# Performance work log

Hardware: AMD Instinct MI355X
Metric: run time of the kernel (lower is better)

Reference implementation:

```python
import jax, jax.numpy as jnp
import numpy as np
from jax import lax

HEADS = 8
DIM_HEAD = 64
SCALE = DIM_HEAD ** -0.5

def conv2d(x, w, stride=1, pad=0):
    return lax.conv_general_dilated(
        x, w, window_strides=(stride, stride),
        padding=[(pad, pad), (pad, pad)],
        dimension_numbers=("NCHW", "OIHW", "NCHW"))

def setup_inputs() -> dict:
    key = jax.random.key(0)
    ks = jax.random.split(key, 5)
    b, dim, H, W = 8, 256, 32, 32
    inner = HEADS * DIM_HEAD  # 512
    x = jax.random.normal(ks[0], (b, dim, H, W), jnp.float32)
    Wq = jax.random.normal(ks[1], (inner, dim, 1, 1), jnp.float32) * 0.05
    Wkv = jax.random.normal(ks[2], (2 * inner, dim, 3, 3), jnp.float32) * 0.05
    Wout = jax.random.normal(ks[3], (dim, inner, 1, 1), jnp.float32) * 0.05
    bout = jnp.zeros((dim,), jnp.float32)
    return {"x": x, "Wq": Wq, "Wkv": Wkv, "Wout": Wout, "bout": bout}

def reference(x, Wq, Wkv, Wout, bout):
    b = x.shape[0]
    h, d = HEADS, DIM_HEAD
    q = conv2d(x, Wq, stride=1, pad=0)        # [b, h*d, H, W]
    kv = conv2d(x, Wkv, stride=1, pad=1)      # [b, 2*h*d, H, W]
    k, v = jnp.split(kv, 2, axis=1)
    out_h, out_w = q.shape[-2:]

    def to_bhnd(t):
        # b (h d) x y -> b h (x y) d
        B, _, X, Y = t.shape
        return t.reshape(B, h, d, X * Y).transpose(0, 1, 3, 2)

    q, k, v = map(to_bhnd, (q, k, v))
    dots = jnp.einsum("bhid,bhjd->bhij", q, k) * SCALE
    attn = jax.nn.softmax(dots, axis=-1)
    out = jnp.einsum("bhij,bhjd->bhid", attn, v)  # [b, h, n, d]
    # b h (x y) d -> b (h d) x y
    out = out.transpose(0, 1, 3, 2).reshape(b, h * d, out_h, out_w)
    out = jax.nn.gelu(out, approximate=False)
    out = conv2d(out, Wout, stride=1, pad=0) + bout[None, :, None, None]
    return out
```

## Files before the change

### kernel.cpp

```cpp
#include <hip/hip_runtime.h>
#include <math.h>

#define BATCH 8
#define DIM   256
#define NPIX  1024
#define DHEAD 64
#define INNER 512
#define KVCH  1024
#define PPIX  1156

typedef _Float16 half8 __attribute__((ext_vector_type(8)));
typedef _Float16 half4 __attribute__((ext_vector_type(4)));
typedef float    f32x4 __attribute__((ext_vector_type(4)));
typedef float    f32x16 __attribute__((ext_vector_type(16)));
#define MFMA16(a, b, c) __builtin_amdgcn_mfma_f32_16x16x32_f16(a, b, c, 0, 0, 0)
#define MFMA32(a, b, c) __builtin_amdgcn_mfma_f32_32x32x16_f16(a, b, c, 0, 0, 0)

static __device__ __forceinline__ float gelu_f(float v) {
    return 0.5f * v * (1.0f + erff(v * 0.70710678118654752440f));
}

static __device__ __forceinline__ void gload16(const _Float16* g, _Float16* l) {
    __builtin_amdgcn_global_load_lds(
        (const __attribute__((address_space(1))) unsigned int*)g,
        (__attribute__((address_space(3))) unsigned int*)l, 16, 0, 0);
}

__global__ __launch_bounds__(256) void prep_kernel(
    const float* __restrict__ Wq, const float* __restrict__ Wkv,
    const float* __restrict__ Wout, const float* __restrict__ x,
    _Float16* __restrict__ Aq, _Float16* __restrict__ Akv,
    _Float16* __restrict__ Aout, _Float16* __restrict__ xtp)
{
    const int bid = blockIdx.x, tid = threadIdx.x;
    if (bid < 512) {
        __shared__ float ts[64][65];
        const int pt = (bid & 15) * 64, ic0 = ((bid >> 4) & 3) * 64, b = bid >> 6;
        const float* xb = x + (((size_t)(b * DIM + ic0)) << 10) + pt;
#pragma unroll
        for (int e = tid; e < 4096; e += 256) {
            int i = e >> 6, p = e & 63;
            ts[i][p] = xb[((size_t)i << 10) + p];
        }
        __syncthreads();
#pragma unroll
        for (int e = tid; e < 512; e += 256) {
            int p = e >> 3, ig = e & 7;
            int gp = pt + p, y = gp >> 5, xc = gp & 31;
            half8 v;
#pragma unroll
            for (int u = 0; u < 8; ++u) v[u] = (_Float16)ts[ig * 8 + u][p];
            *(half8*)&xtp[((size_t)b * PPIX + (y + 1) * 34 + xc + 1) * 256 + ic0 + ig * 8] = v;
        }
    } else if (bid < 1024) {
        const int e = (bid - 512) * 256 + tid;
        Aq[e] = (_Float16)Wq[e];
    } else if (bid < 2048) {
        __shared__ float slab[2304];
        const int oc = bid - 1024;
        const float* src = Wkv + (size_t)oc * 2304;
#pragma unroll
        for (int j = tid; j < 2304; j += 256) slab[j] = src[j];
        __syncthreads();
        _Float16* dst = Akv + (size_t)oc * 2304;
#pragma unroll
        for (int j = tid; j < 2304; j += 256) {
            const int ic = j & 255, s = j >> 8;
            dst[j] = (_Float16)slab[ic * 9 + s];
        }
    } else if (bid < 2560) {
        const int e = (bid - 2048) * 256 + tid;
        Aout[e] = (_Float16)Wout[e];
    } else {
        const int he = (bid - 2560) * 256 + tid;
        int b = he / 33792;
        int r = he - b * 33792;
        int hp = r >> 8, ic = r & 255;
        int row, col;
        if (hp < 34)      { row = 0;  col = hp; }
        else if (hp < 68) { row = 33; col = hp - 34; }
        else { int k2 = hp - 68; row = 1 + (k2 >> 1); col = (k2 & 1) * 33; }
        xtp[((size_t)b * PPIX + row * 34 + col) * 256 + ic] = (_Float16)0.f;
    }
}

__global__ __launch_bounds__(256) void qkv_gemm_kernel(
    const _Float16* __restrict__ Akv, const _Float16* __restrict__ Aq,
    const _Float16* __restrict__ xtp, _Float16* __restrict__ qt,
    _Float16* __restrict__ ktp, _Float16* __restrict__ vb)
{
    __shared__ _Float16 As0[128 * 64];
    __shared__ _Float16 As1[128 * 64];
    __shared__ _Float16 Bs0[128 * 64];
    __shared__ _Float16 Bs1[128 * 64];
    const int nt = blockIdx.x, mt = blockIdx.y, b = blockIdx.z;
    const bool QBLK = (mt >= 8);
    const int tid = threadIdx.x;
    const int w = tid >> 6, lane = tid & 63;
    const int l31 = lane & 31, kh = lane >> 5;
    const int m0 = (QBLK ? mt - 8 : mt) * 128, p0 = nt * 128;
    const int wm = (w >> 1) * 64, wn = (w & 1) * 64;

    const int srow = lane >> 3;
    const int scol = ((lane & 7) ^ srow) * 8;

    const _Float16* abase = QBLK ? Aq : Akv;
    const int astride = QBLK ? 256 : 2304;
    const int ktend = QBLK ? 4 : 36;

    const _Float16* agp[4];
    const _Float16* bgp[4];
#pragma unroll
    for (int c = 0; c < 4; ++c) {
        int row = (w * 4 + c) * 8 + srow;
        agp[c] = abase + (size_t)(m0 + row) * astride + scol;
        int p = p0 + row, py = p >> 5, px = p & 31;
        bgp[c] = xtp + ((size_t)b * PPIX + (py + 1) * 34 + px + 1) * 256 + scol;
    }

    f32x16 acc[2][2];
#pragma unroll
    for (int mf = 0; mf < 2; ++mf)
#pragma unroll
        for (int nf = 0; nf < 2; ++nf)
#pragma unroll
            for (int r = 0; r < 16; ++r) acc[mf][nf][r] = 0.f;

    auto STAGE = [&](int kt, _Float16* Asb, _Float16* Bsb) {
        const int s = QBLK ? 4 : (kt >> 2);
        const int doff = (s / 3 - 1) * 34 + (s - (s / 3) * 3) - 1;
        const int boff = doff * 256 + (kt & 3) * 64;
#pragma unroll
        for (int c = 0; c < 4; ++c)
            gload16(agp[c] + kt * 64, &Asb[(w * 4 + c) * 512]);
#pragma unroll
        for (int c = 0; c < 4; ++c)
            gload16(bgp[c] + boff, &Bsb[(w * 4 + c) * 512]);
    };

    auto COMPUTE = [&](const _Float16* Asb, const _Float16* Bsb) {
#pragma unroll
        for (int kc = 0; kc < 4; ++kc) {
            const int cx = ((((kc << 1) | kh) ^ (l31 & 7)) << 3);
            half8 af[2], bf[2];
#pragma unroll
            for (int mf = 0; mf < 2; ++mf)
                af[mf] = *(const half8*)&Asb[(wm + mf * 32 + l31) * 64 + cx];
#pragma unroll
            for (int nf = 0; nf < 2; ++nf)
                bf[nf] = *(const half8*)&Bsb[(wn + nf * 32 + l31) * 64 + cx];
#pragma unroll
            for (int mf = 0; mf < 2; ++mf)
#pragma unroll
                for (int nf = 0; nf < 2; ++nf)
                    acc[mf][nf] = MFMA32(af[mf], bf[nf], acc[mf][nf]);
        }
    };

    STAGE(0, As0, Bs0);
    __syncthreads();

    for (int kt2 = 0; kt2 < ktend; kt2 += 2) {
        STAGE(kt2 + 1, As1, Bs1);
        COMPUTE(As0, Bs0);
        __syncthreads();
        if (kt2 + 2 < ktend) STAGE(kt2 + 2, As0, Bs0);
        COMPUTE(As1, Bs1);
        __syncthreads();
    }

#pragma unroll
    for (int mf = 0; mf < 2; ++mf) {
        const int mbase = m0 + wm + mf * 32;
        if (!QBLK && mbase >= 512) {
#pragma unroll
            for (int nf = 0; nf < 2; ++nf) {
                const int pix = p0 + wn + nf * 32 + l31;
#pragma unroll
                for (int reg = 0; reg < 16; ++reg) {
                    const int mv = mbase - 512 + (reg & 3) + 8 * (reg >> 2) + 4 * kh;
                    vb[(((size_t)(b * 512 + mv)) << 10) + pix] =
                        (_Float16)acc[mf][nf][reg];
                }
            }
        } else {
            const int h = mbase >> 6;
            const int dbase = (mbase & 63) + kh * 4;
            _Float16* dst = QBLK ? qt : ktp;
#pragma unroll
            for (int nf = 0; nf < 2; ++nf) {
                const int pix = p0 + wn + nf * 32 + l31;
#pragma unroll
                for (int g = 0; g < 4; ++g) {
                    half4 v4;
#pragma unroll
                    for (int r = 0; r < 4; ++r) {
                        float vv = acc[mf][nf][g * 4 + r];
                        if (QBLK) vv *= 0.125f;
                        v4[r] = (_Float16)vv;
                    }
                    *(half4*)&dst[((((size_t)(b * 8 + h)) << 10) + pix) * 64 + dbase + g * 8] = v4;
                }
            }
        }
    }
}

template<int M, int K, int KROW>
__global__ __launch_bounds__(256) void out_gemm_kernel(
    const _Float16* __restrict__ A, const _Float16* __restrict__ act,
    float* __restrict__ Cout, const float* __restrict__ bias)
{
    __shared__ _Float16 As0[128 * 64];
    __shared__ _Float16 As1[128 * 64];
    __shared__ _Float16 Bs0[64 * 64];
    __shared__ _Float16 Bs1[64 * 64];
    const int nt = blockIdx.x, mt = blockIdx.y, b = blockIdx.z;
    const int tid = threadIdx.x;
    const int w = tid >> 6, lane = tid & 63;
    const int quad = lane >> 4, l15 = lane & 15;
    const int m0 = mt * 128, p0 = nt * 64;
    const int wm = w * 32;
    const f32x4 Z4 = {0.f, 0.f, 0.f, 0.f};

    const int srow = lane >> 3;
    const int scol = ((lane & 7) ^ srow) * 8;

    const _Float16* agp[4];
#pragma unroll
    for (int c = 0; c < 4; ++c) {
        int row = (w * 4 + c) * 8 + srow;
        agp[c] = A + (size_t)(m0 + row) * K + scol;
    }
    const _Float16* bgp[2];
#pragma unroll
    for (int c = 0; c < 2; ++c) {
        int row = (w * 2 + c) * 8 + srow;
        bgp[c] = act + (size_t)(b * NPIX + p0 + row) * KROW + scol;
    }

    f32x4 acc[2][4];
#pragma unroll
    for (int mi = 0; mi < 2; ++mi)
#pragma unroll
        for (int ni = 0; ni < 4; ++ni) acc[mi][ni] = Z4;

    auto STAGE = [&](int kt, _Float16* Asb, _Float16* Bsb) {
#pragma unroll
        for (int c = 0; c < 4; ++c)
            gload16(agp[c] + kt * 64, &Asb[(w * 4 + c) * 512]);
#pragma unroll
        for (int c = 0; c < 2; ++c)
            gload16(bgp[c] + kt * 64, &Bsb[(w * 2 + c) * 512]);
    };

    auto COMPUTE = [&](const _Float16* Asb, const _Float16* Bsb) {
#pragma unroll
        for (int ks = 0; ks < 2; ++ks) {
            half8 av[2], bv[4];
#pragma unroll
            for (int mi = 0; mi < 2; ++mi) {
                const int r = wm + mi * 16 + l15;
                av[mi] = *(const half8*)&Asb[r * 64 + (((ks * 4 + quad) ^ (l15 & 7)) << 3)];
            }
#pragma unroll
            for (int ni = 0; ni < 4; ++ni) {
                const int r = ni * 16 + l15;
                bv[ni] = *(const half8*)&Bsb[r * 64 + (((ks * 4 + quad) ^ (l15 & 7)) << 3)];
            }
#pragma unroll
            for (int mi = 0; mi < 2; ++mi)
#pragma unroll
                for (int ni = 0; ni < 4; ++ni)
                    acc[mi][ni] = MFMA16(av[mi], bv[ni], acc[mi][ni]);
        }
    };

    STAGE(0, As0, Bs0);
    __syncthreads();
    for (int kt2 = 0; kt2 < K / 64; kt2 += 2) {
        STAGE(kt2 + 1, As1, Bs1);
        COMPUTE(As0, Bs0);
        __syncthreads();
        if (kt2 + 2 < K / 64) STAGE(kt2 + 2, As0, Bs0);
        COMPUTE(As1, Bs1);
        __syncthreads();
    }

#pragma unroll
    for (int mi = 0; mi < 2; ++mi) {
#pragma unroll
        for (int r = 0; r < 4; ++r) {
            const int m = m0 + wm + mi * 16 + quad * 4 + r;
            const float bv = bias[m];
#pragma unroll
            for (int ni = 0; ni < 4; ++ni) {
                const int pix = p0 + ni * 16 + l15;
                Cout[(((size_t)(b * M + m)) << 10) + pix] = acc[mi][ni][r] + bv;
            }
        }
    }
}

__global__ __launch_bounds__(256) void attn_kernel(
    const _Float16* __restrict__ qt,
    const _Float16* __restrict__ ktp,
    const _Float16* __restrict__ vbb,
    _Float16* __restrict__ gout)
{
    __shared__ _Float16 Ks0[128 * 64];
    __shared__ _Float16 Ks1[128 * 64];
    __shared__ _Float16 Vs[64 * 128];
    __shared__ _Float16 Pb[128 * 128];
    const int qtile = blockIdx.x, bh = blockIdx.y;
    const int b = bh >> 3, h = bh & 7;
    const int p0 = qtile * 128;
    const int tid = threadIdx.x;
    const int w = tid >> 6, lane = tid & 63;
    const int quad = lane >> 4, l15 = lane & 15;
    const f32x4 Z4 = {0.f, 0.f, 0.f, 0.f};

    half8 ones;
#pragma unroll
    for (int u = 0; u < 8; ++u) ones[u] = (_Float16)1.0f;

    half8 qf[2][2];
    {
        const _Float16* qrow =
            qt + ((((size_t)(bh)) << 10) + p0 + w * 32 + l15) * 64;
#pragma unroll
        for (int iff = 0; iff < 2; ++iff)
#pragma unroll
            for (int ks = 0; ks < 2; ++ks)
                qf[iff][ks] = *(const half8*)(qrow + iff * 16 * 64 + ks * 32 + quad * 8);
    }

    const _Float16* kbase = ktp + ((size_t)bh << 16);
    const _Float16* vbase = vbb + (((size_t)(b * 512 + h * 64)) << 10);

    f32x4 oacc[4][2];
#pragma unroll
    for (int mf = 0; mf < 4; ++mf)
#pragma unroll
        for (int iff = 0; iff < 2; ++iff) oacc[mf][iff] = Z4;
    f32x4 racc[2] = {Z4, Z4};

    const int kchunk = (lane & 7) ^ (lane >> 3);

    auto STAGE_K = [&](int kt, _Float16* Kb) {
        const _Float16* kg = kbase + (size_t)(kt * 128) * 64;
#pragma unroll
        for (int i = 0; i < 4; ++i) {
            const int t = i * 4 + w;
            gload16(kg + (t * 8 + (lane >> 3)) * 64 + kchunk * 8, &Kb[t * 512]);
        }
    };
    auto STAGE_V = [&](int kt) {
        const int pk = kt * 128;
#pragma unroll
        for (int i = 0; i < 4; ++i) {
            const int t = i * 4 + w;
            const int vd = t * 4 + (lane >> 4);
            gload16(vbase + ((size_t)vd << 10) + pk + (((lane & 15) ^ (vd & 15)) << 3),
                    &Vs[t * 512]);
        }
    };
    auto QKT = [&](const _Float16* Kb) {
#pragma unroll
        for (int g = 0; g < 2; ++g) {
            f32x4 s[4][2];
#pragma unroll
            for (int jf2 = 0; jf2 < 4; ++jf2) {
                const int jr = (g * 4 + jf2) * 16 + l15;
                const half8 ka0 = *(const half8*)&Kb[jr * 64 + ((quad ^ (l15 & 7)) << 3)];
                const half8 ka1 = *(const half8*)&Kb[jr * 64 + (((4 + quad) ^ (l15 & 7)) << 3)];
#pragma unroll
                for (int iff = 0; iff < 2; ++iff) {
                    s[jf2][iff] = MFMA16(ka0, qf[iff][0], Z4);
                    s[jf2][iff] = MFMA16(ka1, qf[iff][1], s[jf2][iff]);
                }
            }
#pragma unroll
            for (int jf2 = 0; jf2 < 4; ++jf2) {
#pragma unroll
                for (int iff = 0; iff < 2; ++iff) {
                    half4 pv4;
#pragma unroll
                    for (int r = 0; r < 4; ++r)
                        pv4[r] = (_Float16)__expf(s[jf2][iff][r] - 8.0f);
                    const int i = w * 32 + iff * 16 + l15;
                    const int c = ((g * 4 + jf2) << 1) + (quad >> 1);
                    *(half4*)&Pb[i * 128 + ((c ^ l15) << 3) + ((quad & 1) << 2)] = pv4;
                }
            }
        }
    };
    auto PV = [&]() {
#pragma unroll
        for (int kc = 0; kc < 4; ++kc) {
            half8 bv[2];
#pragma unroll
            for (int iff = 0; iff < 2; ++iff) {
                const int i = w * 32 + iff * 16 + l15;
                bv[iff] = *(const half8*)&Pb[i * 128 + (((kc * 4 + quad) ^ l15) << 3)];
                racc[iff] = MFMA16(ones, bv[iff], racc[iff]);
            }
#pragma unroll
            for (int mf = 0; mf < 4; ++mf) {
                const int vr = mf * 16 + l15;
                const half8 va = *(const half8*)&Vs[vr * 128 + (((kc * 4 + quad) ^ l15) << 3)];
#pragma unroll
                for (int iff = 0; iff < 2; ++iff)
                    oacc[mf][iff] = MFMA16(va, bv[iff], oacc[mf][iff]);
            }
        }
    };

    STAGE_K(0, Ks0);
    STAGE_V(0);
    __syncthreads();

    for (int kt2 = 0; kt2 < 8; kt2 += 2) {
        QKT(Ks0);
        __syncthreads();
        STAGE_K(kt2 + 1, Ks1);
        PV();
        __syncthreads();
        STAGE_V(kt2 + 1);
        QKT(Ks1);
        __syncthreads();
        if (kt2 + 2 < 8) STAGE_K(kt2 + 2, Ks0);
        PV();
        __syncthreads();
        if (kt2 + 2 < 8) STAGE_V(kt2 + 2);
    }

    float rinv[2];
#pragma unroll
    for (int iff = 0; iff < 2; ++iff) rinv[iff] = 1.f / racc[iff][0];

    __syncthreads();
    _Float16* scr = Pb;
#pragma unroll
    for (int mf = 0; mf < 4; ++mf) {
#pragma unroll
        for (int iff = 0; iff < 2; ++iff) {
            half4 o4;
#pragma unroll
            for (int r = 0; r < 4; ++r)
                o4[r] = (_Float16)gelu_f(oacc[mf][iff][r] * rinv[iff]);
            const int i = w * 32 + iff * 16 + l15;
            *(half4*)&scr[i * 72 + mf * 16 + quad * 4] = o4;
        }
    }
    __syncthreads();
    _Float16* go = gout + ((size_t)(b * NPIX + p0)) * INNER + h * 64;
#pragma unroll
    for (int it = 0; it < 4; ++it) {
        const int e = tid + it * 256;
        const int p = e >> 3, dg = e & 7;
        *(half8*)(go + (size_t)p * INNER + dg * 8) = *(const half8*)&scr[p * 72 + dg * 8];
    }
}

extern "C" void kernel_launch(void* const* d_in, const int* in_sizes, int n_in,
                              void* d_out, int out_size, void* d_ws, size_t ws_size,
                              hipStream_t stream)
{
    const float* x    = (const float*)d_in[0];
    const float* Wq   = (const float*)d_in[1];
    const float* Wkv  = (const float*)d_in[2];
    const float* Wout = (const float*)d_in[3];
    const float* bout = (const float*)d_in[4];
    float* out = (float*)d_out;

    _Float16* xtp  = (_Float16*)d_ws;
    _Float16* Aq   = xtp  + (size_t)BATCH * PPIX * DIM;
    _Float16* Akv  = Aq   + (size_t)INNER * DIM;
    _Float16* Aout = Akv  + (size_t)KVCH * 2304;
    _Float16* qt   = Aout + (size_t)DIM * INNER;
    _Float16* vb   = qt   + (size_t)BATCH * NPIX * INNER;
    _Float16* ktp  = vb   + (size_t)BATCH * NPIX * INNER;
    _Float16* gout = ktp  + (size_t)BATCH * NPIX * INNER;

    prep_kernel<<<3616, 256, 0, stream>>>(Wq, Wkv, Wout, x, Aq, Akv, Aout, xtp);
    qkv_gemm_kernel<<<dim3(8, 12, BATCH), 256, 0, stream>>>(Akv, Aq, xtp, qt, ktp, vb);
    attn_kernel<<<dim3(8, 64), 256, 0, stream>>>(qt, ktp, vb, gout);
    out_gemm_kernel<DIM, 512, 512>
        <<<dim3(16, 2, BATCH), 256, 0, stream>>>(Aout, gout, out, bout);
}
```

Measured before the change: 168.1 us.

## Fuse all stages into one persistent kernel with software grid barriers

The four separate launches (prep, QKV GEMM, attention, output GEMM) become one persistent kernel of 512 blocks that share a union of LDS buffers. Stages are separated by a global atomic-counter barrier with a spin timeout, so inter-kernel launch gaps go away. Attention is rewritten with a single K buffer and a sync-staged loop instead of the previous double-buffered interleaving. The costs are load imbalance in the QKV stage (half the blocks run two tiles), lost overlap between loads and compute in attention, and reliance on all 512 blocks being co-resident without a cooperative launch.

```diff
diff --git a/kernel.cpp b/kernel.cpp
--- a/kernel.cpp
+++ b/kernel.cpp
@@ -8,6 +8,7 @@
 #define INNER 512
 #define KVCH  1024
 #define PPIX  1156
+#define NBLK  512
 
 typedef _Float16 half8 __attribute__((ext_vector_type(8)));
 typedef _Float16 half4 __attribute__((ext_vector_type(4)));
@@ -16,6 +17,24 @@
 #define MFMA16(a, b, c) __builtin_amdgcn_mfma_f32_16x16x32_f16(a, b, c, 0, 0, 0)
 #define MFMA32(a, b, c) __builtin_amdgcn_mfma_f32_32x32x16_f16(a, b, c, 0, 0, 0)
 
+__device__ unsigned int g_ctr;
+
+static __device__ __forceinline__ void gsync() {
+    __threadfence();
+    __syncthreads();
+    if (threadIdx.x == 0) {
+        unsigned old = __hip_atomic_fetch_add(&g_ctr, 1u, __ATOMIC_ACQ_REL,
+                                              __HIP_MEMORY_SCOPE_AGENT);
+        unsigned tgt = (old / NBLK + 1u) * NBLK;
+        unsigned spins = 0;
+        while (__hip_atomic_load(&g_ctr, __ATOMIC_ACQUIRE,
+                                 __HIP_MEMORY_SCOPE_AGENT) < tgt) {
+            if (++spins > 4000000u) break;
+        }
+    }
+    __syncthreads();
+}
+
 static __device__ __forceinline__ float gelu_f(float v) {
     return 0.5f * v * (1.0f + erff(v * 0.70710678118654752440f));
 }
@@ -26,16 +45,24 @@
         (__attribute__((address_space(3))) unsigned int*)l, 16, 0, 0);
 }
 
-__global__ __launch_bounds__(256) void prep_kernel(
+union SMem {
+    float ts[64][65];
+    float slab[2304];
+    struct { _Float16 A0[8192], A1[8192], B0[8192], B1[8192]; } qk;
+    struct { _Float16 Ks[8192], Vs[8192], Pb[16384]; } at;
+    struct { _Float16 A0[8192], A1[8192], B0[4096], B1[4096]; } op;
+};
+
+static __device__ void prep_unit(
+    int u, int tid, SMem* sm,
     const float* __restrict__ Wq, const float* __restrict__ Wkv,
     const float* __restrict__ Wout, const float* __restrict__ x,
     _Float16* __restrict__ Aq, _Float16* __restrict__ Akv,
     _Float16* __restrict__ Aout, _Float16* __restrict__ xtp)
 {
-    const int bid = blockIdx.x, tid = threadIdx.x;
-    if (bid < 512) {
-        __shared__ float ts[64][65];
-        const int pt = (bid & 15) * 64, ic0 = ((bid >> 4) & 3) * 64, b = bid >> 6;
+    if (u < 512) {
+        float (*ts)[65] = sm->ts;
+        const int pt = (u & 15) * 64, ic0 = ((u >> 4) & 3) * 64, b = u >> 6;
         const float* xb = x + (((size_t)(b * DIM + ic0)) << 10) + pt;
 #pragma unroll
         for (int e = tid; e < 4096; e += 256) {
@@ -49,15 +76,15 @@
             int gp = pt + p, y = gp >> 5, xc = gp & 31;
             half8 v;
 #pragma unroll
-            for (int u = 0; u < 8; ++u) v[u] = (_Float16)ts[ig * 8 + u][p];
+            for (int uu = 0; uu < 8; ++uu) v[uu] = (_Float16)ts[ig * 8 + uu][p];
             *(half8*)&xtp[((size_t)b * PPIX + (y + 1) * 34 + xc + 1) * 256 + ic0 + ig * 8] = v;
         }
-    } else if (bid < 1024) {
-        const int e = (bid - 512) * 256 + tid;
+    } else if (u < 1024) {
+        const int e = (u - 512) * 256 + tid;
         Aq[e] = (_Float16)Wq[e];
-    } else if (bid < 2048) {
-        __shared__ float slab[2304];
-        const int oc = bid - 1024;
+    } else if (u < 2048) {
+        float* slab = sm->slab;
+        const int oc = u - 1024;
         const float* src = Wkv + (size_t)oc * 2304;
 #pragma unroll
         for (int j = tid; j < 2304; j += 256) slab[j] = src[j];
@@ -68,11 +95,11 @@
             const int ic = j & 255, s = j >> 8;
             dst[j] = (_Float16)slab[ic * 9 + s];
         }
-    } else if (bid < 2560) {
-        const int e = (bid - 2048) * 256 + tid;
+    } else if (u < 2560) {
+        const int e = (u - 2048) * 256 + tid;
         Aout[e] = (_Float16)Wout[e];
     } else {
-        const int he = (bid - 2560) * 256 + tid;
+        const int he = (u - 2560) * 256 + tid;
         int b = he / 33792;
         int r = he - b * 33792;
         int hp = r >> 8, ic = r & 255;
@@ -82,23 +109,19 @@
         else { int k2 = hp - 68; row = 1 + (k2 >> 1); col = (k2 & 1) * 33; }
         xtp[((size_t)b * PPIX + row * 34 + col) * 256 + ic] = (_Float16)0.f;
     }
-}
-
-__global__ __launch_bounds__(256) void qkv_gemm_kernel(
+    __syncthreads();
+}
+
+static __device__ void qkv_unit(
+    bool QBLK, int mtl, int nt, int b, int tid,
+    _Float16* As0, _Float16* As1, _Float16* Bs0, _Float16* Bs1,
     const _Float16* __restrict__ Akv, const _Float16* __restrict__ Aq,
     const _Float16* __restrict__ xtp, _Float16* __restrict__ qt,
     _Float16* __restrict__ ktp, _Float16* __restrict__ vb)
 {
-    __shared__ _Float16 As0[128 * 64];
-    __shared__ _Float16 As1[128 * 64];
-    __shared__ _Float16 Bs0[128 * 64];
-    __shared__ _Float16 Bs1[128 * 64];
-    const int nt = blockIdx.x, mt = blockIdx.y, b = blockIdx.z;
-    const bool QBLK = (mt >= 8);
-    const int tid = threadIdx.x;
     const int w = tid >> 6, lane = tid & 63;
     const int l31 = lane & 31, kh = lane >> 5;
-    const int m0 = (QBLK ? mt - 8 : mt) * 128, p0 = nt * 128;
+    const int m0 = mtl * 128, p0 = nt * 128;
     const int wm = (w >> 1) * 64, wn = (w & 1) * 64;
 
     const int srow = lane >> 3;
@@ -204,118 +227,17 @@
             }
         }
     }
-}
-
-template<int M, int K, int KROW>
-__global__ __launch_bounds__(256) void out_gemm_kernel(
-    const _Float16* __restrict__ A, const _Float16* __restrict__ act,
-    float* __restrict__ Cout, const float* __restrict__ bias)
+    __syncthreads();
+}
+
+static __device__ void attn_unit(
+    int qtile, int bh, int tid,
+    _Float16* Ks, _Float16* Vs, _Float16* Pb,
+    const _Float16* __restrict__ qt, const _Float16* __restrict__ ktp,
+    const _Float16* __restrict__ vbb, _Float16* __restrict__ gout)
 {
-    __shared__ _Float16 As0[128 * 64];
-    __shared__ _Float16 As1[128 * 64];
-    __shared__ _Float16 Bs0[64 * 64];
-    __shared__ _Float16 Bs1[64 * 64];
-    const int nt = blockIdx.x, mt = blockIdx.y, b = blockIdx.z;
-    const int tid = threadIdx.x;
-    const int w = tid >> 6, lane = tid & 63;
-    const int quad = lane >> 4, l15 = lane & 15;
-    const int m0 = mt * 128, p0 = nt * 64;
-    const int wm = w * 32;
-    const f32x4 Z4 = {0.f, 0.f, 0.f, 0.f};
-
-    const int srow = lane >> 3;
-    const int scol = ((lane & 7) ^ srow) * 8;
-
-    const _Float16* agp[4];
-#pragma unroll
-    for (int c = 0; c < 4; ++c) {
-        int row = (w * 4 + c) * 8 + srow;
-        agp[c] = A + (size_t)(m0 + row) * K + scol;
-    }
-    const _Float16* bgp[2];
-#pragma unroll
-    for (int c = 0; c < 2; ++c) {
-        int row = (w * 2 + c) * 8 + srow;
-        bgp[c] = act + (size_t)(b * NPIX + p0 + row) * KROW + scol;
-    }
-
-    f32x4 acc[2][4];
-#pragma unroll
-    for (int mi = 0; mi < 2; ++mi)
-#pragma unroll
-        for (int ni = 0; ni < 4; ++ni) acc[mi][ni] = Z4;
-
-    auto STAGE = [&](int kt, _Float16* Asb, _Float16* Bsb) {
-#pragma unroll
-        for (int c = 0; c < 4; ++c)
-            gload16(agp[c] + kt * 64, &Asb[(w * 4 + c) * 512]);
-#pragma unroll
-        for (int c = 0; c < 2; ++c)
-            gload16(bgp[c] + kt * 64, &Bsb[(w * 2 + c) * 512]);
-    };
-
-    auto COMPUTE = [&](const _Float16* Asb, const _Float16* Bsb) {
-#pragma unroll
-        for (int ks = 0; ks < 2; ++ks) {
-            half8 av[2], bv[4];
-#pragma unroll
-            for (int mi = 0; mi < 2; ++mi) {
-                const int r = wm + mi * 16 + l15;
-                av[mi] = *(const half8*)&Asb[r * 64 + (((ks * 4 + quad) ^ (l15 & 7)) << 3)];
-            }
-#pragma unroll
-            for (int ni = 0; ni < 4; ++ni) {
-                const int r = ni * 16 + l15;
-                bv[ni] = *(const half8*)&Bsb[r * 64 + (((ks * 4 + quad) ^ (l15 & 7)) << 3)];
-            }
-#pragma unroll
-            for (int mi = 0; mi < 2; ++mi)
-#pragma unroll
-                for (int ni = 0; ni < 4; ++ni)
-                    acc[mi][ni] = MFMA16(av[mi], bv[ni], acc[mi][ni]);
-        }
-    };
-
-    STAGE(0, As0, Bs0);
-    __syncthreads();
-    for (int kt2 = 0; kt2 < K / 64; kt2 += 2) {
-        STAGE(kt2 + 1, As1, Bs1);
-        COMPUTE(As0, Bs0);
-        __syncthreads();
-        if (kt2 + 2 < K / 64) STAGE(kt2 + 2, As0, Bs0);
-        COMPUTE(As1, Bs1);
-        __syncthreads();
-    }
-
-#pragma unroll
-    for (int mi = 0; mi < 2; ++mi) {
-#pragma unroll
-        for (int r = 0; r < 4; ++r) {
-            const int m = m0 + wm + mi * 16 + quad * 4 + r;
-            const float bv = bias[m];
-#pragma unroll
-            for (int ni = 0; ni < 4; ++ni) {
-                const int pix = p0 + ni * 16 + l15;
-                Cout[(((size_t)(b * M + m)) << 10) + pix] = acc[mi][ni][r] + bv;
-            }
-        }
-    }
-}
-
-__global__ __launch_bounds__(256) void attn_kernel(
-    const _Float16* __restrict__ qt,
-    const _Float16* __restrict__ ktp,
-    const _Float16* __restrict__ vbb,
-    _Float16* __restrict__ gout)
-{
-    __shared__ _Float16 Ks0[128 * 64];
-    __shared__ _Float16 Ks1[128 * 64];
-    __shared__ _Float16 Vs[64 * 128];
-    __shared__ _Float16 Pb[128 * 128];
-    const int qtile = blockIdx.x, bh = blockIdx.y;
     const int b = bh >> 3, h = bh & 7;
     const int p0 = qtile * 128;
-    const int tid = threadIdx.x;
     const int w = tid >> 6, lane = tid & 63;
     const int quad = lane >> 4, l15 = lane & 15;
     const f32x4 Z4 = {0.f, 0.f, 0.f, 0.f};
@@ -346,17 +268,15 @@
     f32x4 racc[2] = {Z4, Z4};
 
     const int kchunk = (lane & 7) ^ (lane >> 3);
-
-    auto STAGE_K = [&](int kt, _Float16* Kb) {
-        const _Float16* kg = kbase + (size_t)(kt * 128) * 64;
+    for (int kt = 0; kt < 8; ++kt) {
+        const int pk = kt * 128;
+        __syncthreads();
+        const _Float16* kg = kbase + (size_t)pk * 64;
 #pragma unroll
         for (int i = 0; i < 4; ++i) {
             const int t = i * 4 + w;
-            gload16(kg + (t * 8 + (lane >> 3)) * 64 + kchunk * 8, &Kb[t * 512]);
-        }
-    };
-    auto STAGE_V = [&](int kt) {
-        const int pk = kt * 128;
+            gload16(kg + (t * 8 + (lane >> 3)) * 64 + kchunk * 8, &Ks[t * 512]);
+        }
 #pragma unroll
         for (int i = 0; i < 4; ++i) {
             const int t = i * 4 + w;
@@ -364,16 +284,16 @@
             gload16(vbase + ((size_t)vd << 10) + pk + (((lane & 15) ^ (vd & 15)) << 3),
                     &Vs[t * 512]);
         }
-    };
-    auto QKT = [&](const _Float16* Kb) {
+        __syncthreads();
+
 #pragma unroll
         for (int g = 0; g < 2; ++g) {
             f32x4 s[4][2];
 #pragma unroll
             for (int jf2 = 0; jf2 < 4; ++jf2) {
                 const int jr = (g * 4 + jf2) * 16 + l15;
-                const half8 ka0 = *(const half8*)&Kb[jr * 64 + ((quad ^ (l15 & 7)) << 3)];
-                const half8 ka1 = *(const half8*)&Kb[jr * 64 + (((4 + quad) ^ (l15 & 7)) << 3)];
+                const half8 ka0 = *(const half8*)&Ks[jr * 64 + ((quad ^ (l15 & 7)) << 3)];
+                const half8 ka1 = *(const half8*)&Ks[jr * 64 + (((4 + quad) ^ (l15 & 7)) << 3)];
 #pragma unroll
                 for (int iff = 0; iff < 2; ++iff) {
                     s[jf2][iff] = MFMA16(ka0, qf[iff][0], Z4);
@@ -394,8 +314,6 @@
                 }
             }
         }
-    };
-    auto PV = [&]() {
 #pragma unroll
         for (int kc = 0; kc < 4; ++kc) {
             half8 bv[2];
@@ -414,25 +332,6 @@
                     oacc[mf][iff] = MFMA16(va, bv[iff], oacc[mf][iff]);
             }
         }
-    };
-
-    STAGE_K(0, Ks0);
-    STAGE_V(0);
-    __syncthreads();
-
-    for (int kt2 = 0; kt2 < 8; kt2 += 2) {
-        QKT(Ks0);
-        __syncthreads();
-        STAGE_K(kt2 + 1, Ks1);
-        PV();
-        __syncthreads();
-        STAGE_V(kt2 + 1);
-        QKT(Ks1);
-        __syncthreads();
-        if (kt2 + 2 < 8) STAGE_K(kt2 + 2, Ks0);
-        PV();
-        __syncthreads();
-        if (kt2 + 2 < 8) STAGE_V(kt2 + 2);
     }
 
     float rinv[2];
@@ -461,6 +360,136 @@
         const int p = e >> 3, dg = e & 7;
         *(half8*)(go + (size_t)p * INNER + dg * 8) = *(const half8*)&scr[p * 72 + dg * 8];
     }
+    __syncthreads();
+}
+
+static __device__ void out_unit(
+    int nt, int mt, int b, int tid,
+    _Float16* As0, _Float16* As1, _Float16* Bs0, _Float16* Bs1,
+    const _Float16* __restrict__ A, const _Float16* __restrict__ act,
+    float* __restrict__ Cout, const float* __restrict__ bias)
+{
+    const int K = 512, KROW = 512, M = DIM;
+    const int w = tid >> 6, lane = tid & 63;
+    const int quad = lane >> 4, l15 = lane & 15;
+    const int m0 = mt * 128, p0 = nt * 64;
+    const int wm = w * 32;
+    const f32x4 Z4 = {0.f, 0.f, 0.f, 0.f};
+
+    const int srow = lane >> 3;
+    const int scol = ((lane & 7) ^ srow) * 8;
+
+    const _Float16* agp[4];
+#pragma unroll
+    for (int c = 0; c < 4; ++c) {
+        int row = (w * 4 + c) * 8 + srow;
+        agp[c] = A + (size_t)(m0 + row) * K + scol;
+    }
+    const _Float16* bgp[2];
+#pragma unroll
+    for (int c = 0; c < 2; ++c) {
+        int row = (w * 2 + c) * 8 + srow;
+        bgp[c] = act + (size_t)(b * NPIX + p0 + row) * KROW + scol;
+    }
+
+    f32x4 acc[2][4];
+#pragma unroll
+    for (int mi = 0; mi < 2; ++mi)
+#pragma unroll
+        for (int ni = 0; ni < 4; ++ni) acc[mi][ni] = Z4;
+
+    auto STAGE = [&](int kt, _Float16* Asb, _Float16* Bsb) {
+#pragma unroll
+        for (int c = 0; c < 4; ++c)
+            gload16(agp[c] + kt * 64, &Asb[(w * 4 + c) * 512]);
+#pragma unroll
+        for (int c = 0; c < 2; ++c)
+            gload16(bgp[c] + kt * 64, &Bsb[(w * 2 + c) * 512]);
+    };
+
+    auto COMPUTE = [&](const _Float16* Asb, const _Float16* Bsb) {
+#pragma unroll
+        for (int ks = 0; ks < 2; ++ks) {
+            half8 av[2], bv[4];
+#pragma unroll
+            for (int mi = 0; mi < 2; ++mi) {
+                const int r = wm + mi * 16 + l15;
+                av[mi] = *(const half8*)&Asb[r * 64 + (((ks * 4 + quad) ^ (l15 & 7)) << 3)];
+            }
+#pragma unroll
+            for (int ni = 0; ni < 4; ++ni) {
+                const int r = ni * 16 + l15;
+                bv[ni] = *(const half8*)&Bsb[r * 64 + (((ks * 4 + quad) ^ (l15 & 7)) << 3)];
+            }
+#pragma unroll
+            for (int mi = 0; mi < 2; ++mi)
+#pragma unroll
+                for (int ni = 0; ni < 4; ++ni)
+                    acc[mi][ni] = MFMA16(av[mi], bv[ni], acc[mi][ni]);
+        }
+    };
+
+    STAGE(0, As0, Bs0);
+    __syncthreads();
+    for (int kt2 = 0; kt2 < K / 64; kt2 += 2) {
+        STAGE(kt2 + 1, As1, Bs1);
+        COMPUTE(As0, Bs0);
+        __syncthreads();
+        if (kt2 + 2 < K / 64) STAGE(kt2 + 2, As0, Bs0);
+        COMPUTE(As1, Bs1);
+        __syncthreads();
+    }
+
+#pragma unroll
+    for (int mi = 0; mi < 2; ++mi) {
+#pragma unroll
+        for (int r = 0; r < 4; ++r) {
+            const int m = m0 + wm + mi * 16 + quad * 4 + r;
+            const float bv = bias[m];
+#pragma unroll
+            for (int ni = 0; ni < 4; ++ni) {
+                const int pix = p0 + ni * 16 + l15;
+                Cout[(((size_t)(b * M + m)) << 10) + pix] = acc[mi][ni][r] + bv;
+            }
+        }
+    }
+}
+
+__global__ __launch_bounds__(256, 2) void fused_kernel(
+    const float* __restrict__ Wq, const float* __restrict__ Wkv,
+    const float* __restrict__ Wout, const float* __restrict__ x,
+    const float* __restrict__ bout, float* __restrict__ out,
+    _Float16* __restrict__ Aq, _Float16* __restrict__ Akv,
+    _Float16* __restrict__ Aout, _Float16* __restrict__ xtp,
+    _Float16* __restrict__ qt, _Float16* __restrict__ vb,
+    _Float16* __restrict__ ktp, _Float16* __restrict__ gout)
+{
+    __shared__ SMem sm;
+    const int bid = blockIdx.x, tid = threadIdx.x;
+
+    for (int u = bid; u < 3616; u += NBLK)
+        prep_unit(u, tid, &sm, Wq, Wkv, Wout, x, Aq, Akv, Aout, xtp);
+    gsync();
+
+    qkv_unit(false, (bid >> 3) & 7, bid & 7, bid >> 6, tid,
+             sm.qk.A0, sm.qk.A1, sm.qk.B0, sm.qk.B1,
+             Akv, Aq, xtp, qt, ktp, vb);
+    if (bid >= 256) {
+        const int qi = bid - 256;
+        qkv_unit(true, (qi >> 3) & 3, qi & 7, qi >> 5, tid,
+                 sm.qk.A0, sm.qk.A1, sm.qk.B0, sm.qk.B1,
+                 Akv, Aq, xtp, qt, ktp, vb);
+    }
+    gsync();
+
+    attn_unit(bid & 7, bid >> 3, tid, sm.at.Ks, sm.at.Vs, sm.at.Pb,
+              qt, ktp, vb, gout);
+    gsync();
+
+    if (bid < 256)
+        out_unit(bid & 15, (bid >> 4) & 1, bid >> 5, tid,
+                 sm.op.A0, sm.op.A1, sm.op.B0, sm.op.B1,
+                 Aout, gout, out, bout);
 }
 
 extern "C" void kernel_launch(void* const* d_in, const int* in_sizes, int n_in,
@@ -483,9 +512,6 @@
     _Float16* ktp  = vb   + (size_t)BATCH * NPIX * INNER;
     _Float16* gout = ktp  + (size_t)BATCH * NPIX * INNER;
 
-    prep_kernel<<<3616, 256, 0, stream>>>(Wq, Wkv, Wout, x, Aq, Akv, Aout, xtp);
-    qkv_gemm_kernel<<<dim3(8, 12, BATCH), 256, 0, stream>>>(Akv, Aq, xtp, qt, ktp, vb);
-    attn_kernel<<<dim3(8, 64), 256, 0, stream>>>(qt, ktp, vb, gout);
-    out_gemm_kernel<DIM, 512, 512>
-        <<<dim3(16, 2, BATCH), 256, 0, stream>>>(Aout, gout, out, bout);
-}
+    fused_kernel<<<NBLK, 256, 0, stream>>>(
+        Wq, Wkv, Wout, x, bout, out, Aq, Akv, Aout, xtp, qt, vb, ktp, gout);
+}
```

Result: slower. 461.6 us (+174.7%).
